# Kernel tuning notes

Measured on AMD Instinct MI355X. Metric: run time of the kernel, lower is better.

Reference implementation:

```python
import jax, jax.numpy as jnp
import numpy as np
import math

D_MODEL = 1024
NUM_HEADS = 16
D_K = D_MODEL // NUM_HEADS
THETA = 10000.0
NEG_INF = 1.0e6  # module uses -1e6, not -inf


def _rope_tables(seq_len):
    pair_idx = jnp.arange(0, D_K, 2, dtype=jnp.float32)
    inv_freq = 1.0 / (THETA ** (pair_idx / D_K))
    pos = jnp.arange(seq_len, dtype=jnp.float32)
    angles = jnp.outer(pos, inv_freq)  # (S, D_K//2)
    return jnp.cos(angles), jnp.sin(angles)


def _apply_rope(x, cos, sin):
    # x: (B, H, S, D_K); cos/sin: (S, D_K//2)
    xe = x[..., 0::2]
    xo = x[..., 1::2]
    oe = xe * cos - xo * sin
    oo = xe * sin + xo * cos
    return jnp.stack([oe, oo], axis=-1).reshape(x.shape)


def setup_inputs() -> dict:
    key = jax.random.key(0)
    k0, k1, k2, k3, k4 = jax.random.split(key, 5)
    B, S = 2, 2048
    x = jax.random.normal(k0, (B, S, D_MODEL), dtype=jnp.float32)
    scale = 0.02
    wq = jax.random.normal(k1, (D_MODEL, D_MODEL), dtype=jnp.float32) * scale
    wk = jax.random.normal(k2, (D_MODEL, D_MODEL), dtype=jnp.float32) * scale
    wv = jax.random.normal(k3, (D_MODEL, D_MODEL), dtype=jnp.float32) * scale
    wo = jax.random.normal(k4, (D_MODEL, D_MODEL), dtype=jnp.float32) * scale
    return {"x": x, "wq": wq, "wk": wk, "wv": wv, "wo": wo}


def reference(x, wq, wk, wv, wo):
    B, S, _ = x.shape
    q = x @ wq.T
    k = x @ wk.T
    v = x @ wv.T
    # (B, S, H, d_k) -> (B, H, S, d_k)
    q = q.reshape(B, S, NUM_HEADS, D_K).transpose(0, 2, 1, 3)
    k = k.reshape(B, S, NUM_HEADS, D_K).transpose(0, 2, 1, 3)
    v = v.reshape(B, S, NUM_HEADS, D_K).transpose(0, 2, 1, 3)
    cos, sin = _rope_tables(S)
    q = _apply_rope(q, cos, sin)
    k = _apply_rope(k, cos, sin)
    scores = jnp.einsum("bhqd,bhkd->bhqk", q, k) / math.sqrt(D_K)
    causal = jnp.tril(jnp.ones((S, S), dtype=bool))
    scores = jnp.where(causal, scores, -NEG_INF)
    attn = jax.nn.softmax(scores, axis=-1)
    out = jnp.einsum("bhqk,bhkd->bhqd", attn, v)
    out = out.transpose(0, 2, 1, 3).reshape(B, S, D_MODEL)
    return out @ wo.T
```

## Files before the change

### kernel.cpp

```cpp
#include <hip/hip_runtime.h>

typedef __attribute__((ext_vector_type(8))) __bf16 bf16x8;
typedef __attribute__((ext_vector_type(8))) _Float16 f16x8;
typedef __attribute__((ext_vector_type(4))) float f32x4;
typedef __attribute__((ext_vector_type(8))) unsigned short u16x8;

#define MFMA_BF16(a, b, c) __builtin_amdgcn_mfma_f32_16x16x32_bf16((a), (b), (c), 0, 0, 0)
#define MFMA_F16(a, b, c)  __builtin_amdgcn_mfma_f32_16x16x32_f16((a), (b), (c), 0, 0, 0)
#define LOG2E 1.44269504088896340736f

__device__ __forceinline__ float b2f(unsigned short u) {
    union { unsigned int i; float f; } v; v.i = ((unsigned int)u) << 16; return v.f;
}
__device__ __forceinline__ unsigned short f2bf(float f) {
    union { float f; unsigned int i; } v; v.f = f;
    unsigned int u = v.i;
    return (unsigned short)((u + 0x7fffu + ((u >> 16) & 1u)) >> 16);
}

__device__ __forceinline__ void gl_lds16(const void* g, void* l) {
    __builtin_amdgcn_global_load_lds(
        (const __attribute__((address_space(1))) void*)g,
        (__attribute__((address_space(3))) void*)l,
        16, 0, 0);
}

__global__ __launch_bounds__(256) void cvt_all(const float* __restrict__ x,
                                               const float* __restrict__ wq,
                                               const float* __restrict__ wk,
                                               const float* __restrict__ wv,
                                               const float* __restrict__ wo,
                                               unsigned short* __restrict__ xb,
                                               unsigned short* __restrict__ wqb,
                                               unsigned short* __restrict__ wkb,
                                               unsigned short* __restrict__ wvb,
                                               unsigned short* __restrict__ wob) {
    int id = blockIdx.x * 256 + threadIdx.x;
    const float* src; unsigned short* dst; size_t off;
    if (id < 524288)      { src = x;  dst = xb;  off = (size_t)id * 8; }
    else if (id < 655360) { src = wq; dst = wqb; off = (size_t)(id - 524288) * 8; }
    else if (id < 786432) { src = wk; dst = wkb; off = (size_t)(id - 655360) * 8; }
    else if (id < 917504) { src = wv; dst = wvb; off = (size_t)(id - 786432) * 8; }
    else                  { src = wo; dst = wob; off = (size_t)(id - 917504) * 8; }
    float4 a = *(const float4*)(src + off);
    float4 b = *(const float4*)(src + off + 4);
    u16x8 o;
    o[0] = f2bf(a.x); o[1] = f2bf(a.y); o[2] = f2bf(a.z); o[3] = f2bf(a.w);
    o[4] = f2bf(b.x); o[5] = f2bf(b.y); o[6] = f2bf(b.z); o[7] = f2bf(b.w);
    *(u16x8*)(dst + off) = o;
}

template <int MODE>
__device__ __forceinline__ void gemm128_bt(const unsigned short* __restrict__ A,
                                           const unsigned short* __restrict__ B,
                                           void* __restrict__ Cv,
                                           int m0, int n0, int ldc,
                                           unsigned short* As, unsigned short* Bs) {
    const int tid = threadIdx.x;
    const int w = tid >> 6, lane = tid & 63;
    const int quad = lane >> 4, l15 = lane & 15;
    const int wm = w & 1, wn = w >> 1;

    f32x4 acc[4][4];
#pragma unroll
    for (int mt = 0; mt < 4; ++mt)
#pragma unroll
        for (int nt = 0; nt < 4; ++nt) acc[mt][nt] = f32x4{0.f, 0.f, 0.f, 0.f};

    for (int k0 = 0; k0 < 1024; k0 += 32) {
        __syncthreads();
#pragma unroll
        for (int i = 0; i < 2; ++i) {
            int L = (w * 2 + i) * 64 + lane;
            int r = L >> 2;
            int c = (L & 3) ^ ((r >> 1) & 3);
            gl_lds16(A + (size_t)(m0 + r) * 1024 + k0 + c * 8, As + L * 8);
            gl_lds16(B + (size_t)(n0 + r) * 1024 + k0 + c * 8, Bs + L * 8);
        }
        __syncthreads();

        bf16x8 af[4], bfr[4];
#pragma unroll
        for (int mt = 0; mt < 4; ++mt) {
            int row = wm * 64 + mt * 16 + l15;
            af[mt] = *(const bf16x8*)(As + row * 32 + (quad ^ ((row >> 1) & 3)) * 8);
        }
#pragma unroll
        for (int nt = 0; nt < 4; ++nt) {
            int row = wn * 64 + nt * 16 + l15;
            bfr[nt] = *(const bf16x8*)(Bs + row * 32 + (quad ^ ((row >> 1) & 3)) * 8);
        }
#pragma unroll
        for (int mt = 0; mt < 4; ++mt)
#pragma unroll
            for (int nt = 0; nt < 4; ++nt)
                acc[mt][nt] = MFMA_BF16(af[mt], bfr[nt], acc[mt][nt]);
    }

#pragma unroll
    for (int mt = 0; mt < 4; ++mt) {
        int grow = m0 + wm * 64 + mt * 16 + quad * 4;
#pragma unroll
        for (int nt = 0; nt < 4; ++nt) {
            int gcol = n0 + wn * 64 + nt * 16 + l15;
#pragma unroll
            for (int r = 0; r < 4; ++r) {
                float val = acc[mt][nt][r];
                size_t idx = (size_t)(grow + r) * ldc + gcol;
                if constexpr (MODE == 0) {
                    ((unsigned short*)Cv)[idx] = f2bf(val);
                } else if constexpr (MODE == 1) {
                    ((float*)Cv)[idx] = val;
                } else {
                    _Float16 hv = (_Float16)val;
                    ((unsigned short*)Cv)[idx] = __builtin_bit_cast(unsigned short, hv);
                }
            }
        }
    }
}

__global__ __launch_bounds__(256) void gemm_qkv(const unsigned short* __restrict__ X,
                                                const unsigned short* __restrict__ Wq,
                                                const unsigned short* __restrict__ Wk,
                                                const unsigned short* __restrict__ Wv,
                                                unsigned short* __restrict__ Qo,
                                                unsigned short* __restrict__ Ko,
                                                unsigned short* __restrict__ Vt) {
    __shared__ unsigned short As[128 * 32];
    __shared__ unsigned short Bs[128 * 32];
    int y = blockIdx.y;
    if (y < 16) {
        int sel = y >> 3;
        int m0 = blockIdx.x * 128;
        int n0 = (y & 7) * 128;
        const unsigned short* B = sel ? Wk : Wq;
        unsigned short* C = sel ? Ko : Qo;
        gemm128_bt<0>(X, B, C, m0, n0, 1024, As, Bs);
    } else {
        int m0 = (y & 7) * 128;
        int n0 = blockIdx.x * 128;
        gemm128_bt<2>(Wv, X, Vt, m0, n0, 4096, As, Bs);
    }
}

__global__ __launch_bounds__(256) void gemm_out(const unsigned short* __restrict__ A,
                                                const unsigned short* __restrict__ Wo,
                                                float* __restrict__ C) {
    __shared__ unsigned short As[128 * 32];
    __shared__ unsigned short Bs[128 * 32];
    gemm128_bt<1>(A, Wo, C, blockIdx.x * 128, blockIdx.y * 128, 1024, As, Bs);
}

__global__ __launch_bounds__(256) void rope_qk(unsigned short* __restrict__ Q,
                                               unsigned short* __restrict__ K) {
    int id = blockIdx.x * 256 + threadIdx.x;
    int tsel = id >> 21;
    int rgt = id & 0x1FFFFF;
    int row = rgt >> 9;
    int p = rgt & 511;
    int pp = p & 31;
    int col = (p >> 5) * 64 + pp * 2;
    float pos = (float)(row & 2047);
    float inv_freq = exp2f(-0.41524101186092029f * (float)pp);
    float ang = pos * inv_freq;
    float sn = __sinf(ang);
    float cs = __cosf(ang);
    unsigned short* buf = tsel ? K : Q;
    float scale = tsel ? 1.0f : (0.125f * LOG2E);
    size_t base = (size_t)row * 1024 + col;
    float xe = b2f(buf[base]), xo = b2f(buf[base + 1]);
    buf[base]     = f2bf((xe * cs - xo * sn) * scale);
    buf[base + 1] = f2bf((xe * sn + xo * cs) * scale);
}

#define FBODY(KB, MASKED)                                                               \
    {                                                                                   \
        const int kb_ = (KB);                                                           \
        const unsigned short* Kc = Ks[kb_ & 1];                                         \
        const unsigned short* Vc = Vs[kb_ & 1];                                         \
        f32x4 sc[4];                                                                    \
        _Pragma("unroll")                                                               \
        for (int nt = 0; nt < 4; ++nt) {                                                \
            int row = nt * 16 + l15;                                                    \
            int cof = (quad ^ (row & 7)) * 8;                                           \
            bf16x8 kf0 = *(const bf16x8*)(Kc + row * 64 + cof);                         \
            bf16x8 kf1 = *(const bf16x8*)(Kc + row * 64 + (cof ^ 32));                  \
            f32x4 z = f32x4{0.f, 0.f, 0.f, 0.f};                                        \
            sc[nt] = MFMA_BF16(qf0, kf0, z);                                            \
            sc[nt] = MFMA_BF16(qf1, kf1, sc[nt]);                                       \
        }                                                                               \
        unsigned short* Pw = Ps[w];                                                     \
        _Pragma("unroll")                                                               \
        for (int nt = 0; nt < 4; ++nt) {                                                \
            float e[4];                                                                 \
            _Pragma("unroll")                                                           \
            for (int r = 0; r < 4; ++r) {                                               \
                float ev = exp2f(sc[nt][r]);                                            \
                if (MASKED) {                                                           \
                    int kpos = kb_ * 64 + nt * 16 + l15;                                \
                    int qpos = qpos0 + quad * 4 + r;                                    \
                    ev = (kpos > qpos) ? 0.f : ev;                                      \
                }                                                                       \
                e[r] = ev;                                                              \
            }                                                                           \
            unsigned pk01 = __builtin_bit_cast(unsigned,                                \
                                __builtin_amdgcn_cvt_pkrtz(e[0], e[1]));                \
            unsigned pk23 = __builtin_bit_cast(unsigned,                                \
                                __builtin_amdgcn_cvt_pkrtz(e[2], e[3]));                \
            int col = nt * 16 + l15;                                                    \
            Pw[(quad * 4 + 0) * 72 + col] = (unsigned short)pk01;                       \
            Pw[(quad * 4 + 1) * 72 + col] = (unsigned short)(pk01 >> 16);               \
            Pw[(quad * 4 + 2) * 72 + col] = (unsigned short)pk23;                       \
            Pw[(quad * 4 + 3) * 72 + col] = (unsigned short)(pk23 >> 16);               \
        }                                                                               \
        __asm__ volatile("s_waitcnt lgkmcnt(0)" ::: "memory");                          \
        f16x8 pf0 = *(const f16x8*)(Pw + l15 * 72 + quad * 8);                          \
        f16x8 pf1 = *(const f16x8*)(Pw + l15 * 72 + 32 + quad * 8);                     \
        lacc = MFMA_F16(pf0, ones, lacc);                                               \
        lacc = MFMA_F16(pf1, ones, lacc);                                               \
        _Pragma("unroll")                                                               \
        for (int nt = 0; nt < 4; ++nt) {                                                \
            int row = nt * 16 + l15;                                                    \
            int cof = (quad ^ (row & 7)) * 8;                                           \
            f16x8 vf0 = *(const f16x8*)(Vc + row * 64 + cof);                           \
            f16x8 vf1 = *(const f16x8*)(Vc + row * 64 + (cof ^ 32));                    \
            accO[nt] = MFMA_F16(pf0, vf0, accO[nt]);                                    \
            accO[nt] = MFMA_F16(pf1, vf1, accO[nt]);                                    \
        }                                                                               \
    }

__global__ __launch_bounds__(256) void flash_attn(const unsigned short* __restrict__ Q,
                                                  const unsigned short* __restrict__ Kb,
                                                  const unsigned short* __restrict__ Vt,
                                                  unsigned short* __restrict__ O) {
    int id = blockIdx.x;
    int xcd = id & 7;
    int sl = id >> 3;
    int rr = sl >> 5;
    int j  = sl & 31;
    int qt;
    if (rr == 0)      qt = j;
    else if (rr == 1) qt = 31 - j;
    else if (rr == 2) qt = (j + 16) & 31;
    else              qt = 31 - ((j + 16) & 31);
    int bh = xcd + 8 * rr;
    int b = bh >> 4, h = bh & 15;
    int tid = threadIdx.x, w = tid >> 6, lane = tid & 63;
    int quad = lane >> 4, l15 = lane & 15;
    int qrow0 = b * 2048 + qt * 64 + w * 16;
    int qpos0 = qt * 64 + w * 16;

    __shared__ unsigned short Ks[2][64 * 64];
    __shared__ unsigned short Vs[2][64 * 64];
    __shared__ unsigned short Ps[4][16 * 72];

    bf16x8 qf0, qf1;
    {
        const unsigned short* qp = Q + (size_t)(qrow0 + l15) * 1024 + h * 64 + quad * 8;
        qf0 = *(const bf16x8*)qp;
        qf1 = *(const bf16x8*)(qp + 32);
    }
    f16x8 ones;
#pragma unroll
    for (int jj = 0; jj < 8; ++jj) ones[jj] = (_Float16)1.0f;

    int L0 = w * 128 + lane;
    int L1 = L0 + 64;
    int r0 = L0 >> 3, c0s = (L0 & 7) ^ (r0 & 7);
    int r1 = L1 >> 3, c1s = (L1 & 7) ^ (r1 & 7);
    const unsigned short* Kg0 = Kb + (size_t)(b * 2048 + r0) * 1024 + h * 64 + c0s * 8;
    const unsigned short* Kg1 = Kb + (size_t)(b * 2048 + r1) * 1024 + h * 64 + c1s * 8;
    const unsigned short* Vg0 = Vt + (size_t)(h * 64 + r0) * 4096 + b * 2048 + c0s * 8;
    const unsigned short* Vg1 = Vt + (size_t)(h * 64 + r1) * 4096 + b * 2048 + c1s * 8;

    f32x4 accO[4];
#pragma unroll
    for (int nt = 0; nt < 4; ++nt) accO[nt] = f32x4{0.f, 0.f, 0.f, 0.f};
    f32x4 lacc = f32x4{0.f, 0.f, 0.f, 0.f};

    gl_lds16(Kg0, Ks[0] + L0 * 8);
    gl_lds16(Kg1, Ks[0] + L1 * 8);
    gl_lds16(Vg0, Vs[0] + L0 * 8);
    gl_lds16(Vg1, Vs[0] + L1 * 8);

    for (int kb = 0; kb < qt; ++kb) {
        __syncthreads();
        int bi = (kb + 1) & 1;
        size_t ko = (size_t)(kb + 1) * 64 * 1024;
        size_t vo = (size_t)(kb + 1) * 64;
        gl_lds16(Kg0 + ko, Ks[bi] + L0 * 8);
        gl_lds16(Kg1 + ko, Ks[bi] + L1 * 8);
        gl_lds16(Vg0 + vo, Vs[bi] + L0 * 8);
        gl_lds16(Vg1 + vo, Vs[bi] + L1 * 8);
        FBODY(kb, 0)
    }
    __syncthreads();
    FBODY(qt, 1)

    float inv[4];
#pragma unroll
    for (int r = 0; r < 4; ++r) inv[r] = 1.0f / lacc[r];
#pragma unroll
    for (int nt = 0; nt < 4; ++nt)
#pragma unroll
        for (int r = 0; r < 4; ++r)
            O[(size_t)(qrow0 + quad * 4 + r) * 1024 + h * 64 + nt * 16 + l15] =
                f2bf(accO[nt][r] * inv[r]);
}

extern "C" void kernel_launch(void* const* d_in, const int* in_sizes, int n_in,
                              void* d_out, int out_size, void* d_ws, size_t ws_size,
                              hipStream_t stream) {
    (void)in_sizes; (void)n_in; (void)out_size; (void)ws_size;
    const float* x  = (const float*)d_in[0];
    const float* wq = (const float*)d_in[1];
    const float* wk = (const float*)d_in[2];
    const float* wv = (const float*)d_in[3];
    const float* wo = (const float*)d_in[4];
    float* out = (float*)d_out;

    const size_t T = (size_t)4096 * 1024;
    const size_t W = (size_t)1024 * 1024;
    unsigned short* Q   = (unsigned short*)d_ws;
    unsigned short* K   = Q + T;
    unsigned short* Vt  = K + T;
    unsigned short* AO  = Vt + T;
    unsigned short* xb  = AO + T;
    unsigned short* wqb = xb + T;
    unsigned short* wkb = wqb + W;
    unsigned short* wvb = wkb + W;
    unsigned short* wob = wvb + W;

    cvt_all  <<<dim3(4096),   256, 0, stream>>>(x, wq, wk, wv, wo, xb, wqb, wkb, wvb, wob);
    gemm_qkv <<<dim3(32, 24), 256, 0, stream>>>(xb, wqb, wkb, wvb, Q, K, Vt);
    rope_qk  <<<dim3(16384),  256, 0, stream>>>(Q, K);
    flash_attn<<<dim3(1024),  256, 0, stream>>>(Q, K, Vt, AO);
    gemm_out <<<dim3(32, 8),  256, 0, stream>>>(AO, wob, out);
}
```

Baseline: 199.1 us.

## Fuse RoPE into QKV GEMM epilogue and fold Q scale into weights

Applies rotary embedding inside the Q/K projection GEMM epilogue, using a lane shuffle to get the paired element, and removes the separate rope kernel with its read-modify-write pass over Q and K. The softmax scale is folded into the bf16 conversion of wq. Flash attention drops its double-buffered K/V LDS staging for a single buffer with synchronous load-then-compute, and AO reuses the xb workspace. The single buffer gives up the overlap of global loads with compute, and the epilogue now evaluates sin/cos per output element.

```diff
diff --git a/kernel.cpp b/kernel.cpp
--- a/kernel.cpp
+++ b/kernel.cpp
@@ -8,6 +8,7 @@
 #define MFMA_BF16(a, b, c) __builtin_amdgcn_mfma_f32_16x16x32_bf16((a), (b), (c), 0, 0, 0)
 #define MFMA_F16(a, b, c)  __builtin_amdgcn_mfma_f32_16x16x32_f16((a), (b), (c), 0, 0, 0)
 #define LOG2E 1.44269504088896340736f
+#define QSCALE 0.18033688011112042f
 
 __device__ __forceinline__ float b2f(unsigned short u) {
     union { unsigned int i; float f; } v; v.i = ((unsigned int)u) << 16; return v.f;
@@ -36,17 +37,17 @@
                                                unsigned short* __restrict__ wvb,
                                                unsigned short* __restrict__ wob) {
     int id = blockIdx.x * 256 + threadIdx.x;
-    const float* src; unsigned short* dst; size_t off;
+    const float* src; unsigned short* dst; size_t off; float scl = 1.0f;
     if (id < 524288)      { src = x;  dst = xb;  off = (size_t)id * 8; }
-    else if (id < 655360) { src = wq; dst = wqb; off = (size_t)(id - 524288) * 8; }
+    else if (id < 655360) { src = wq; dst = wqb; off = (size_t)(id - 524288) * 8; scl = QSCALE; }
     else if (id < 786432) { src = wk; dst = wkb; off = (size_t)(id - 655360) * 8; }
     else if (id < 917504) { src = wv; dst = wvb; off = (size_t)(id - 786432) * 8; }
     else                  { src = wo; dst = wob; off = (size_t)(id - 917504) * 8; }
     float4 a = *(const float4*)(src + off);
     float4 b = *(const float4*)(src + off + 4);
     u16x8 o;
-    o[0] = f2bf(a.x); o[1] = f2bf(a.y); o[2] = f2bf(a.z); o[3] = f2bf(a.w);
-    o[4] = f2bf(b.x); o[5] = f2bf(b.y); o[6] = f2bf(b.z); o[7] = f2bf(b.w);
+    o[0] = f2bf(a.x * scl); o[1] = f2bf(a.y * scl); o[2] = f2bf(a.z * scl); o[3] = f2bf(a.w * scl);
+    o[4] = f2bf(b.x * scl); o[5] = f2bf(b.y * scl); o[6] = f2bf(b.z * scl); o[7] = f2bf(b.w * scl);
     *(u16x8*)(dst + off) = o;
 }
 
@@ -97,6 +98,14 @@
                 acc[mt][nt] = MFMA_BF16(af[mt], bfr[nt], acc[mt][nt]);
     }
 
+    float invf[4], sgn = 0.f;
+    if constexpr (MODE == 3) {
+        sgn = (l15 & 1) ? 1.0f : -1.0f;
+#pragma unroll
+        for (int nt = 0; nt < 4; ++nt)
+            invf[nt] = exp2f(-0.41524101186092029f * (float)((nt * 16 + l15) >> 1));
+    }
+
 #pragma unroll
     for (int mt = 0; mt < 4; ++mt) {
         int grow = m0 + wm * 64 + mt * 16 + quad * 4;
@@ -111,9 +120,15 @@
                     ((unsigned short*)Cv)[idx] = f2bf(val);
                 } else if constexpr (MODE == 1) {
                     ((float*)Cv)[idx] = val;
-                } else {
+                } else if constexpr (MODE == 2) {
                     _Float16 hv = (_Float16)val;
                     ((unsigned short*)Cv)[idx] = __builtin_bit_cast(unsigned short, hv);
+                } else {
+                    float p = __shfl_xor(val, 1);
+                    float pos = (float)((grow + r) & 2047);
+                    float ang = pos * invf[nt];
+                    float out = val * __cosf(ang) + sgn * p * __sinf(ang);
+                    ((unsigned short*)Cv)[idx] = f2bf(out);
                 }
             }
         }
@@ -136,7 +151,7 @@
         int n0 = (y & 7) * 128;
         const unsigned short* B = sel ? Wk : Wq;
         unsigned short* C = sel ? Ko : Qo;
-        gemm128_bt<0>(X, B, C, m0, n0, 1024, As, Bs);
+        gemm128_bt<3>(X, B, C, m0, n0, 1024, As, Bs);
     } else {
         int m0 = (y & 7) * 128;
         int n0 = blockIdx.x * 128;
@@ -152,40 +167,16 @@
     gemm128_bt<1>(A, Wo, C, blockIdx.x * 128, blockIdx.y * 128, 1024, As, Bs);
 }
 
-__global__ __launch_bounds__(256) void rope_qk(unsigned short* __restrict__ Q,
-                                               unsigned short* __restrict__ K) {
-    int id = blockIdx.x * 256 + threadIdx.x;
-    int tsel = id >> 21;
-    int rgt = id & 0x1FFFFF;
-    int row = rgt >> 9;
-    int p = rgt & 511;
-    int pp = p & 31;
-    int col = (p >> 5) * 64 + pp * 2;
-    float pos = (float)(row & 2047);
-    float inv_freq = exp2f(-0.41524101186092029f * (float)pp);
-    float ang = pos * inv_freq;
-    float sn = __sinf(ang);
-    float cs = __cosf(ang);
-    unsigned short* buf = tsel ? K : Q;
-    float scale = tsel ? 1.0f : (0.125f * LOG2E);
-    size_t base = (size_t)row * 1024 + col;
-    float xe = b2f(buf[base]), xo = b2f(buf[base + 1]);
-    buf[base]     = f2bf((xe * cs - xo * sn) * scale);
-    buf[base + 1] = f2bf((xe * sn + xo * cs) * scale);
-}
-
 #define FBODY(KB, MASKED)                                                               \
     {                                                                                   \
         const int kb_ = (KB);                                                           \
-        const unsigned short* Kc = Ks[kb_ & 1];                                         \
-        const unsigned short* Vc = Vs[kb_ & 1];                                         \
         f32x4 sc[4];                                                                    \
         _Pragma("unroll")                                                               \
         for (int nt = 0; nt < 4; ++nt) {                                                \
             int row = nt * 16 + l15;                                                    \
             int cof = (quad ^ (row & 7)) * 8;                                           \
-            bf16x8 kf0 = *(const bf16x8*)(Kc + row * 64 + cof);                         \
-            bf16x8 kf1 = *(const bf16x8*)(Kc + row * 64 + (cof ^ 32));                  \
+            bf16x8 kf0 = *(const bf16x8*)(Ks + row * 64 + cof);                         \
+            bf16x8 kf1 = *(const bf16x8*)(Ks + row * 64 + (cof ^ 32));                  \
             f32x4 z = f32x4{0.f, 0.f, 0.f, 0.f};                                        \
             sc[nt] = MFMA_BF16(qf0, kf0, z);                                            \
             sc[nt] = MFMA_BF16(qf1, kf1, sc[nt]);                                       \
@@ -223,8 +214,8 @@
         for (int nt = 0; nt < 4; ++nt) {                                                \
             int row = nt * 16 + l15;                                                    \
             int cof = (quad ^ (row & 7)) * 8;                                           \
-            f16x8 vf0 = *(const f16x8*)(Vc + row * 64 + cof);                           \
-            f16x8 vf1 = *(const f16x8*)(Vc + row * 64 + (cof ^ 32));                    \
+            f16x8 vf0 = *(const f16x8*)(Vs + row * 64 + cof);                           \
+            f16x8 vf1 = *(const f16x8*)(Vs + row * 64 + (cof ^ 32));                    \
             accO[nt] = MFMA_F16(pf0, vf0, accO[nt]);                                    \
             accO[nt] = MFMA_F16(pf1, vf1, accO[nt]);                                    \
         }                                                                               \
@@ -251,8 +242,8 @@
     int qrow0 = b * 2048 + qt * 64 + w * 16;
     int qpos0 = qt * 64 + w * 16;
 
-    __shared__ unsigned short Ks[2][64 * 64];
-    __shared__ unsigned short Vs[2][64 * 64];
+    __shared__ unsigned short Ks[64 * 64];
+    __shared__ unsigned short Vs[64 * 64];
     __shared__ unsigned short Ps[4][16 * 72];
 
     bf16x8 qf0, qf1;
@@ -279,24 +270,23 @@
     for (int nt = 0; nt < 4; ++nt) accO[nt] = f32x4{0.f, 0.f, 0.f, 0.f};
     f32x4 lacc = f32x4{0.f, 0.f, 0.f, 0.f};
 
-    gl_lds16(Kg0, Ks[0] + L0 * 8);
-    gl_lds16(Kg1, Ks[0] + L1 * 8);
-    gl_lds16(Vg0, Vs[0] + L0 * 8);
-    gl_lds16(Vg1, Vs[0] + L1 * 8);
-
-    for (int kb = 0; kb < qt; ++kb) {
+    for (int kb = 0; kb <= qt; ++kb) {
         __syncthreads();
-        int bi = (kb + 1) & 1;
-        size_t ko = (size_t)(kb + 1) * 64 * 1024;
-        size_t vo = (size_t)(kb + 1) * 64;
-        gl_lds16(Kg0 + ko, Ks[bi] + L0 * 8);
-        gl_lds16(Kg1 + ko, Ks[bi] + L1 * 8);
-        gl_lds16(Vg0 + vo, Vs[bi] + L0 * 8);
-        gl_lds16(Vg1 + vo, Vs[bi] + L1 * 8);
-        FBODY(kb, 0)
-    }
-    __syncthreads();
-    FBODY(qt, 1)
+        {
+            size_t ko = (size_t)kb * 64 * 1024;
+            size_t vo = (size_t)kb * 64;
+            gl_lds16(Kg0 + ko, Ks + L0 * 8);
+            gl_lds16(Kg1 + ko, Ks + L1 * 8);
+            gl_lds16(Vg0 + vo, Vs + L0 * 8);
+            gl_lds16(Vg1 + vo, Vs + L1 * 8);
+        }
+        __syncthreads();
+        if (kb < qt) {
+            FBODY(kb, 0)
+        } else {
+            FBODY(kb, 1)
+        }
+    }
 
     float inv[4];
 #pragma unroll
@@ -325,8 +315,8 @@
     unsigned short* Q   = (unsigned short*)d_ws;
     unsigned short* K   = Q + T;
     unsigned short* Vt  = K + T;
-    unsigned short* AO  = Vt + T;
-    unsigned short* xb  = AO + T;
+    unsigned short* xb  = Vt + T;
+    unsigned short* AO  = xb;
     unsigned short* wqb = xb + T;
     unsigned short* wkb = wqb + W;
     unsigned short* wvb = wkb + W;
@@ -334,7 +324,6 @@
 
     cvt_all  <<<dim3(4096),   256, 0, stream>>>(x, wq, wk, wv, wo, xb, wqb, wkb, wvb, wob);
     gemm_qkv <<<dim3(32, 24), 256, 0, stream>>>(xb, wqb, wkb, wvb, Q, K, Vt);
-    rope_qk  <<<dim3(16384),  256, 0, stream>>>(Q, K);
     flash_attn<<<dim3(1024),  256, 0, stream>>>(Q, K, Vt, AO);
     gemm_out <<<dim3(32, 8),  256, 0, stream>>>(AO, wob, out);
 }
```

Measured after the change: 187.3 us. 5.9% less time.
